# Performance work log

Measured on AMD Instinct MI355X. Metric: run time of the kernel, lower is better.

## Reference

```python
import jax, jax.numpy as jnp
import numpy as np

B, LQ, LKV, D = 8, 2048, 2048, 1024

def setup_inputs() -> dict:
    key = jax.random.key(0)
    k1, k2, k3, k4, k5, k6, k7 = jax.random.split(key, 7)
    s = 1.0 / np.sqrt(D)
    return {
        "query": jax.random.normal(k1, (B, LQ, D), jnp.float32),
        "key": jax.random.normal(k2, (B, LKV, D), jnp.float32),
        "value": jax.random.normal(k3, (B, LKV, D), jnp.float32),
        "Wq": jax.random.uniform(k4, (D, D), jnp.float32, -s, s),
        "bq": jax.random.uniform(k5, (D,), jnp.float32, -s, s),
        "Wk": jax.random.uniform(k6, (D, D), jnp.float32, -s, s),
        "bk": jax.random.uniform(k7, (D,), jnp.float32, -s, s),
        "scale_factor": 32,
        "dropout_p": 0,
    }

def reference(query, key, value, Wq, bq, Wk, bk, scale_factor, dropout_p):
    # q/k linear projections (torch Linear: x @ W^T + b); v is used raw per the source
    q = jnp.einsum("bld,ed->ble", query, Wq) + bq
    k = jnp.einsum("bld,ed->ble", key, Wk) + bk
    scores = jnp.einsum("bqd,bkd->bqk", q, k) / jnp.float32(scale_factor)
    attn = jax.nn.softmax(scores, axis=-1)
    # dropout_p == 0 -> identity (deterministic baseline)
    return jnp.einsum("bqk,bkd->bqd", attn, value)
```

## Files before the change

### kernel.cpp

```cpp
#include <hip/hip_runtime.h>

typedef __bf16 bf16;
typedef __attribute__((ext_vector_type(4))) __bf16 bf16x4;
typedef __attribute__((ext_vector_type(8))) __bf16 bf16x8;
typedef __attribute__((ext_vector_type(4))) float f32x4;

__device__ __forceinline__ void gload_lds16(const void* g, void* l) {
  __builtin_amdgcn_global_load_lds(
      (const __attribute__((address_space(1))) unsigned int*)(unsigned long long)g,
      (__attribute__((address_space(3))) unsigned int*)(unsigned long long)l,
      16, 0, 0);
}

__global__ void cast_f32_bf16(const float* __restrict__ in, bf16* __restrict__ out, int n4) {
  int i = blockIdx.x * blockDim.x + threadIdx.x;
  if (i >= n4) return;
  float4 v = reinterpret_cast<const float4*>(in)[i];
  bf16x4 o;
  o[0] = (bf16)v.x; o[1] = (bf16)v.y; o[2] = (bf16)v.z; o[3] = (bf16)v.w;
  reinterpret_cast<bf16x4*>(out)[i] = o;
}

__global__ void transpose_cast(const float* __restrict__ V, bf16* __restrict__ VT,
                               int rows, int cols) {
  __shared__ bf16 tile[64][65];
  const int b = blockIdx.z;
  const float* Vb = V + (long)b * rows * cols;
  bf16* VTb = VT + (long)b * rows * cols;
  const int d0 = blockIdx.x * 64;
  const int k0 = blockIdx.y * 64;
  const int t = threadIdx.x;
  const int r = t >> 4;
  const int c4 = (t & 15) * 4;
#pragma unroll
  for (int p = 0; p < 4; ++p) {
    float4 v = *reinterpret_cast<const float4*>(&Vb[(long)(k0 + p * 16 + r) * cols + d0 + c4]);
    tile[p * 16 + r][c4 + 0] = (bf16)v.x;
    tile[p * 16 + r][c4 + 1] = (bf16)v.y;
    tile[p * 16 + r][c4 + 2] = (bf16)v.z;
    tile[p * 16 + r][c4 + 3] = (bf16)v.w;
  }
  __syncthreads();
#pragma unroll
  for (int p = 0; p < 4; ++p) {
    const int dd = p * 16 + r;
    bf16x4 o;
    o[0] = tile[c4 + 0][dd];
    o[1] = tile[c4 + 1][dd];
    o[2] = tile[c4 + 2][dd];
    o[3] = tile[c4 + 3][dd];
    *reinterpret_cast<bf16x4*>(&VTb[(long)(d0 + dd) * rows + k0 + c4]) = o;
  }
}

__global__ void softmax_rows(bf16* __restrict__ S) {
  const long row = blockIdx.x;
  bf16* p = S + row * 2048;
  const int t = threadIdx.x;
  const int wid = t >> 6;
  const int lane = t & 63;
  bf16x8 v = *reinterpret_cast<bf16x8*>(p + t * 8);
  float f[8];
  float m = -3.0e38f;
#pragma unroll
  for (int j = 0; j < 8; ++j) { f[j] = (float)v[j]; m = fmaxf(m, f[j]); }
#pragma unroll
  for (int off = 32; off >= 1; off >>= 1) m = fmaxf(m, __shfl_xor(m, off));
  __shared__ float redm[4], reds[4];
  if (lane == 0) redm[wid] = m;
  __syncthreads();
  m = fmaxf(fmaxf(redm[0], redm[1]), fmaxf(redm[2], redm[3]));
  float s = 0.f;
#pragma unroll
  for (int j = 0; j < 8; ++j) { f[j] = __expf(f[j] - m); s += f[j]; }
#pragma unroll
  for (int off = 32; off >= 1; off >>= 1) s += __shfl_xor(s, off);
  if (lane == 0) reds[wid] = s;
  __syncthreads();
  s = reds[0] + reds[1] + reds[2] + reds[3];
  const float inv = 1.0f / s;
  bf16x8 o;
#pragma unroll
  for (int j = 0; j < 8; ++j) o[j] = (bf16)(f[j] * inv);
  *reinterpret_cast<bf16x8*>(p + t * 8) = o;
}


#define BARRIER __builtin_amdgcn_s_barrier()
#define LGKM0                                              \
  do {                                                     \
    asm volatile("s_waitcnt lgkmcnt(0)" ::: "memory");     \
    __builtin_amdgcn_sched_barrier(0);                     \
  } while (0)
#define VM0                                                \
  do {                                                     \
    asm volatile("s_waitcnt vmcnt(0)" ::: "memory");       \
    __builtin_amdgcn_sched_barrier(0);                     \
  } while (0)

#define STAGE_A(buf, ko)                                        \
  {                                                             \
    bf16* l_ = ldsd + (buf) * 32768;                            \
    const bf16* g_ = gA + (ko);                                 \
    gload_lds16(g_, l_);                                        \
    gload_lds16(g_ + rK64, l_ + 4096);                          \
    gload_lds16(g_ + rK128, l_ + 8192);                         \
    gload_lds16(g_ + rK128 + rK64, l_ + 12288);                 \
  }
#define STAGE_B(buf, ko)                                        \
  {                                                             \
    bf16* l_ = ldsd + (buf) * 32768 + 16384;                    \
    const bf16* g_ = gB + (ko);                                 \
    gload_lds16(g_, l_);                                        \
    gload_lds16(g_ + rK64, l_ + 4096);                          \
    gload_lds16(g_ + rK128, l_ + 8192);                         \
    gload_lds16(g_ + rK128 + rK64, l_ + 12288);                 \
  }

#define LOADA(buf, mq)                                                        \
  {                                                                           \
    const bf16* p_ = aBase + (buf) * 32768 + (mq) * 4096;                     \
    _Pragma("unroll") for (int m_ = 0; m_ < 4; ++m_) {                        \
      a[m_][0] = *reinterpret_cast<const bf16x8*>(p_ + m_ * 1024 + pk0);      \
      a[m_][1] = *reinterpret_cast<const bf16x8*>(p_ + m_ * 1024 + pk1);      \
    }                                                                         \
  }
#define LOADB(buf, nq)                                                        \
  {                                                                           \
    const bf16* p_ = bBase + (buf) * 32768 + (nq) * 2048;                     \
    _Pragma("unroll") for (int n_ = 0; n_ < 2; ++n_) {                        \
      b[(nq) * 2 + n_][0] = *reinterpret_cast<const bf16x8*>(p_ + n_ * 1024 + pk0); \
      b[(nq) * 2 + n_][1] = *reinterpret_cast<const bf16x8*>(p_ + n_ * 1024 + pk1); \
    }                                                                         \
  }

#define MFMAQ(mq, nq)                                                         \
  _Pragma("unroll") for (int m_ = 0; m_ < 4; ++m_)                            \
  _Pragma("unroll") for (int n_ = 0; n_ < 2; ++n_)                            \
  _Pragma("unroll") for (int ks_ = 0; ks_ < 2; ++ks_)                         \
      acc[(mq) * 4 + m_][(nq) * 2 + n_] =                                     \
          __builtin_amdgcn_mfma_f32_16x16x32_bf16(                            \
              a[m_][ks_], b[(nq) * 2 + n_][ks_],                              \
              acc[(mq) * 4 + m_][(nq) * 2 + n_], 0, 0, 0);

template <int MODE>
__global__ __launch_bounds__(512, 2)
void gemm_bt(const bf16* __restrict__ A, const bf16* __restrict__ Bm,
             const float* __restrict__ bias, void* __restrict__ Cvoid,
             const int* __restrict__ scale_ptr,
             int M, int N, int K, long sA, long sB, long sC) {
  __shared__ bf16 lds[2][2][2][128][64];
  const int t = threadIdx.x;
  const int lane = t & 63;
  const int wid = t >> 6;
  const int wm = wid >> 2;
  const int wn = wid & 3;
  (void)M;

  const int gx = gridDim.x, gy = gridDim.y;
  const int nwg = gx * gy * gridDim.z;
  int id = blockIdx.x + gx * (blockIdx.y + gy * blockIdx.z);
  {
    const int cpx = nwg >> 3;
    id = (id & 7) * cpx + (id >> 3);
  }
  const int bx = id % gx;
  const int by = (id / gx) % gy;
  const int bz = id / (gx * gy);

  const bf16* Ab = A + (long)bz * sA;
  const bf16* Bb = Bm + (long)bz * sB;
  const int tile_m = by * 256;
  const int tile_n = bx * 256;

  const int srow = t >> 3;
  const int skc = t & 7;
  const int soff = ((skc ^ (srow & 7)) << 3);
  const bf16* gA = Ab + (long)(tile_m + srow) * K + soff;
  const bf16* gB = Bb + (long)(tile_n + srow) * K + soff;
  const long rK64 = (long)K << 6;
  const long rK128 = (long)K << 7;
  bf16* const ldsd = &lds[0][0][0][0][0] + wid * 512;

  const int frow = lane & 15;
  const int pk0 = (((lane >> 4) ^ (lane & 7))) << 3;
  const int pk1 = (((4 | (lane >> 4)) ^ (lane & 7))) << 3;
  const bf16* aBase = &lds[0][0][wm][frow][0];
  const bf16* bBase = &lds[0][1][wn >> 1][(wn & 1) * 64 + frow][0];

  bf16x8 a[4][2], b[4][2];
  f32x4 acc[8][4] = {};

  STAGE_A(0, 0)
  STAGE_B(0, 0)
  VM0;
  BARRIER;

  const int NK = K >> 6;
  int c = 0;
  for (int kt = 0; kt < NK - 1; ++kt, c ^= 1) {
    const long ko = (long)(kt + 1) << 6;
    LOADA(c, 0)
    LOADB(c, 0)
    STAGE_A(c ^ 1, ko)
    BARRIER;
    LGKM0;
    __builtin_amdgcn_s_setprio(1);
    MFMAQ(0, 0)
    __builtin_amdgcn_s_setprio(0);
    BARRIER;
    LOADB(c, 1)
    STAGE_B(c ^ 1, ko)
    BARRIER;
    LGKM0;
    __builtin_amdgcn_s_setprio(1);
    MFMAQ(0, 1)
    __builtin_amdgcn_s_setprio(0);
    BARRIER;
    LOADA(c, 1)
    BARRIER;
    LGKM0;
    __builtin_amdgcn_s_setprio(1);
    MFMAQ(1, 0)
    __builtin_amdgcn_s_setprio(0);
    BARRIER;
    VM0;
    BARRIER;
    __builtin_amdgcn_s_setprio(1);
    MFMAQ(1, 1)
    __builtin_amdgcn_s_setprio(0);
  }
  LOADA(c, 0)
  LOADB(c, 0)
  LOADB(c, 1)
  MFMAQ(0, 0)
  MFMAQ(0, 1)
  LOADA(c, 1)
  MFMAQ(1, 0)
  MFMAQ(1, 1)

  float scl = 1.0f;
  if (MODE == 1) {
    const int iv = scale_ptr[0];
    const float fv = __int_as_float(iv);
    const float sv = (iv > 0 && iv < (1 << 20)) ? (float)iv : fv;
    scl = 1.0f / sv;
  }
  const int rb = tile_m + wm * 128 + ((lane >> 4) << 2);
  const int cb = tile_n + wn * 64 + (lane & 15);
  if (MODE == 2) {
    float* C = reinterpret_cast<float*>(Cvoid) + (long)bz * sC;
#pragma unroll
    for (int mf = 0; mf < 8; ++mf)
#pragma unroll
      for (int nf = 0; nf < 4; ++nf)
#pragma unroll
        for (int r = 0; r < 4; ++r)
          C[(long)(rb + mf * 16 + r) * N + (cb + nf * 16)] = acc[mf][nf][r];
  } else {
    bf16* C = reinterpret_cast<bf16*>(Cvoid) + (long)bz * sC;
#pragma unroll
    for (int nf = 0; nf < 4; ++nf) {
      const int col = cb + nf * 16;
      const float bv = (MODE == 0) ? bias[col] : 0.0f;
#pragma unroll
      for (int mf = 0; mf < 8; ++mf)
#pragma unroll
        for (int r = 0; r < 4; ++r)
          C[(long)(rb + mf * 16 + r) * N + col] = (bf16)(acc[mf][nf][r] * scl + bv);
    }
  }
}

extern "C" void kernel_launch(void* const* d_in, const int* in_sizes, int n_in,
                              void* d_out, int out_size, void* d_ws, size_t ws_size,
                              hipStream_t stream) {
  (void)in_sizes; (void)n_in; (void)out_size; (void)ws_size;
  const float* query = (const float*)d_in[0];
  const float* key   = (const float*)d_in[1];
  const float* value = (const float*)d_in[2];
  const float* Wq    = (const float*)d_in[3];
  const float* bq    = (const float*)d_in[4];
  const float* Wk    = (const float*)d_in[5];
  const float* bk    = (const float*)d_in[6];
  const int*   scale = (const int*)d_in[7];

  const int L = 2048, D = 1024;
  char* ws = (char*)d_ws;
  bf16* q_cast = (bf16*)ws;
  bf16* k_cast = q_cast + (long)16384 * 1024;
  bf16* S      = q_cast;
  bf16* Qp     = (bf16*)(ws + (size_t)67108864);
  bf16* Kp     = (bf16*)(ws + (size_t)100663296);
  bf16* VT     = (bf16*)(ws + (size_t)134217728);
  bf16* Wqb    = (bf16*)(ws + (size_t)167772160);
  bf16* Wkb    = (bf16*)(ws + (size_t)169869312);

  cast_f32_bf16<<<16384, 256, 0, stream>>>(query, q_cast, 4194304);
  cast_f32_bf16<<<16384, 256, 0, stream>>>(key,   k_cast, 4194304);
  cast_f32_bf16<<<1024,  256, 0, stream>>>(Wq, Wqb, 262144);
  cast_f32_bf16<<<1024,  256, 0, stream>>>(Wk, Wkb, 262144);
  transpose_cast<<<dim3(16, 32, 8), 256, 0, stream>>>(value, VT, 2048, 1024);

  gemm_bt<0><<<dim3(4, 64, 1), 512, 0, stream>>>(q_cast, Wqb, bq, Qp, nullptr,
                                                 16384, 1024, 1024, 0, 0, 0);
  gemm_bt<0><<<dim3(4, 64, 1), 512, 0, stream>>>(k_cast, Wkb, bk, Kp, nullptr,
                                                 16384, 1024, 1024, 0, 0, 0);
  gemm_bt<1><<<dim3(8, 8, 8), 512, 0, stream>>>(Qp, Kp, nullptr, S, scale,
                                                2048, 2048, 1024,
                                                (long)L * D, (long)L * D, (long)L * L);
  softmax_rows<<<16384, 256, 0, stream>>>(S);
  gemm_bt<2><<<dim3(4, 8, 8), 512, 0, stream>>>(S, VT, nullptr, d_out, nullptr,
                                                2048, 1024, 2048,
                                                (long)L * L, (long)D * L, (long)L * D);
}
```

Before: 289.0 us.

## Split GEMM K-tile into two 32-wide halves with finer-grained load/compute pipelining

Restructures the bf16 GEMM main loop so each 64-wide K tile is staged and consumed as two 32-wide halves for A and B separately, using partial vmcnt waits so later stages keep loading while earlier halves are computed. LDS layout changes from a swizzled 64-column layout to an unswizzled [8][256][32] layout, and fragment loads become one bf16x8 per operand per half. This aims to overlap global-to-LDS traffic with MFMA work and drop the full vmcnt(0) stall. The price is more barriers and the loss of the XOR swizzle, which may bring back LDS bank conflicts.

```diff
diff --git a/kernel.cpp b/kernel.cpp
--- a/kernel.cpp
+++ b/kernel.cpp
@@ -92,56 +92,38 @@
     asm volatile("s_waitcnt lgkmcnt(0)" ::: "memory");     \
     __builtin_amdgcn_sched_barrier(0);                     \
   } while (0)
+#define VM4                                                \
+  do {                                                     \
+    asm volatile("s_waitcnt vmcnt(4)" ::: "memory");       \
+    __builtin_amdgcn_sched_barrier(0);                     \
+  } while (0)
 #define VM0                                                \
   do {                                                     \
     asm volatile("s_waitcnt vmcnt(0)" ::: "memory");       \
     __builtin_amdgcn_sched_barrier(0);                     \
   } while (0)
 
-#define STAGE_A(buf, ko)                                        \
+#define STAGE(buf, op, kh, g_)                                  \
   {                                                             \
-    bf16* l_ = ldsd + (buf) * 32768;                            \
-    const bf16* g_ = gA + (ko);                                 \
-    gload_lds16(g_, l_);                                        \
-    gload_lds16(g_ + rK64, l_ + 4096);                          \
-    gload_lds16(g_ + rK128, l_ + 8192);                         \
-    gload_lds16(g_ + rK128 + rK64, l_ + 12288);                 \
-  }
-#define STAGE_B(buf, ko)                                        \
-  {                                                             \
-    bf16* l_ = ldsd + (buf) * 32768 + 16384;                    \
-    const bf16* g_ = gB + (ko);                                 \
-    gload_lds16(g_, l_);                                        \
-    gload_lds16(g_ + rK64, l_ + 4096);                          \
-    gload_lds16(g_ + rK128, l_ + 8192);                         \
-    gload_lds16(g_ + rK128 + rK64, l_ + 12288);                 \
-  }
-
-#define LOADA(buf, mq)                                                        \
-  {                                                                           \
-    const bf16* p_ = aBase + (buf) * 32768 + (mq) * 4096;                     \
-    _Pragma("unroll") for (int m_ = 0; m_ < 4; ++m_) {                        \
-      a[m_][0] = *reinterpret_cast<const bf16x8*>(p_ + m_ * 1024 + pk0);      \
-      a[m_][1] = *reinterpret_cast<const bf16x8*>(p_ + m_ * 1024 + pk1);      \
-    }                                                                         \
-  }
-#define LOADB(buf, nq)                                                        \
-  {                                                                           \
-    const bf16* p_ = bBase + (buf) * 32768 + (nq) * 2048;                     \
-    _Pragma("unroll") for (int n_ = 0; n_ < 2; ++n_) {                        \
-      b[(nq) * 2 + n_][0] = *reinterpret_cast<const bf16x8*>(p_ + n_ * 1024 + pk0); \
-      b[(nq) * 2 + n_][1] = *reinterpret_cast<const bf16x8*>(p_ + n_ * 1024 + pk1); \
-    }                                                                         \
-  }
-
-#define MFMAQ(mq, nq)                                                         \
-  _Pragma("unroll") for (int m_ = 0; m_ < 4; ++m_)                            \
-  _Pragma("unroll") for (int n_ = 0; n_ < 2; ++n_)                            \
-  _Pragma("unroll") for (int ks_ = 0; ks_ < 2; ++ks_)                         \
-      acc[(mq) * 4 + m_][(nq) * 2 + n_] =                                     \
-          __builtin_amdgcn_mfma_f32_16x16x32_bf16(                            \
-              a[m_][ks_], b[(nq) * 2 + n_][ks_],                              \
-              acc[(mq) * 4 + m_][(nq) * 2 + n_], 0, 0, 0);
+    bf16* l_ = ldsw + (((buf) * 2 + (op)) * 2 + (kh)) * 8192;   \
+    gload_lds16((g_), l_);                                      \
+    gload_lds16((g_) + rK128, l_ + 4096);                       \
+  }
+
+#define LOADA(buf, kh, mq)                                                     \
+  _Pragma("unroll") for (int m_ = 0; m_ < 4; ++m_)                             \
+      a[m_] = *reinterpret_cast<const bf16x8*>(                                \
+          aB + ((buf) * 4 + (kh)) * 8192 + (mq) * 2048 + m_ * 512);
+#define LOADB(buf, kh)                                                         \
+  _Pragma("unroll") for (int n_ = 0; n_ < 4; ++n_)                             \
+      b[n_] = *reinterpret_cast<const bf16x8*>(                                \
+          bB + ((buf) * 4 + 2 + (kh)) * 8192 + n_ * 512);
+
+#define MFMAP(mq)                                                              \
+  _Pragma("unroll") for (int m_ = 0; m_ < 4; ++m_)                             \
+  _Pragma("unroll") for (int n_ = 0; n_ < 4; ++n_)                             \
+      acc[(mq) * 4 + m_][n_] = __builtin_amdgcn_mfma_f32_16x16x32_bf16(        \
+          a[m_], b[n_], acc[(mq) * 4 + m_][n_], 0, 0, 0);
 
 template <int MODE>
 __global__ __launch_bounds__(512, 2)
@@ -149,7 +131,7 @@
              const float* __restrict__ bias, void* __restrict__ Cvoid,
              const int* __restrict__ scale_ptr,
              int M, int N, int K, long sA, long sB, long sC) {
-  __shared__ bf16 lds[2][2][2][128][64];
+  __shared__ bf16 lds[8][256][32];
   const int t = threadIdx.x;
   const int lane = t & 63;
   const int wid = t >> 6;
@@ -173,71 +155,85 @@
   const int tile_m = by * 256;
   const int tile_n = bx * 256;
 
-  const int srow = t >> 3;
-  const int skc = t & 7;
-  const int soff = ((skc ^ (srow & 7)) << 3);
+  const int srow = t >> 2;
+  const int soff = (t & 3) * 8;
   const bf16* gA = Ab + (long)(tile_m + srow) * K + soff;
   const bf16* gB = Bb + (long)(tile_n + srow) * K + soff;
-  const long rK64 = (long)K << 6;
   const long rK128 = (long)K << 7;
-  bf16* const ldsd = &lds[0][0][0][0][0] + wid * 512;
+  bf16* const ldsw = &lds[0][0][0] + wid * 512;
 
   const int frow = lane & 15;
-  const int pk0 = (((lane >> 4) ^ (lane & 7))) << 3;
-  const int pk1 = (((4 | (lane >> 4)) ^ (lane & 7))) << 3;
-  const bf16* aBase = &lds[0][0][wm][frow][0];
-  const bf16* bBase = &lds[0][1][wn >> 1][(wn & 1) * 64 + frow][0];
-
-  bf16x8 a[4][2], b[4][2];
+  const int fko = (lane >> 4) * 8;
+  const bf16* aB = &lds[0][0][0] + (wm * 128 + frow) * 32 + fko;
+  const bf16* bB = &lds[0][0][0] + (wn * 64 + frow) * 32 + fko;
+
+  bf16x8 a[4], b[4];
   f32x4 acc[8][4] = {};
 
-  STAGE_A(0, 0)
-  STAGE_B(0, 0)
-  VM0;
+  STAGE(0, 0, 0, gA)
+  STAGE(0, 1, 0, gB)
+  STAGE(0, 0, 1, gA + 32)
+  STAGE(0, 1, 1, gB + 32)
+  VM4;
   BARRIER;
 
   const int NK = K >> 6;
   int c = 0;
   for (int kt = 0; kt < NK - 1; ++kt, c ^= 1) {
     const long ko = (long)(kt + 1) << 6;
-    LOADA(c, 0)
     LOADB(c, 0)
-    STAGE_A(c ^ 1, ko)
+    LOADA(c, 0, 0)
+    STAGE(c ^ 1, 0, 0, gA + ko)
     BARRIER;
     LGKM0;
     __builtin_amdgcn_s_setprio(1);
-    MFMAQ(0, 0)
+    MFMAP(0)
     __builtin_amdgcn_s_setprio(0);
     BARRIER;
-    LOADB(c, 1)
-    STAGE_B(c ^ 1, ko)
+    LOADA(c, 0, 1)
+    STAGE(c ^ 1, 1, 0, gB + ko)
+    VM4;
     BARRIER;
     LGKM0;
     __builtin_amdgcn_s_setprio(1);
-    MFMAQ(0, 1)
+    MFMAP(1)
     __builtin_amdgcn_s_setprio(0);
     BARRIER;
-    LOADA(c, 1)
+    LOADB(c, 1)
+    LOADA(c, 1, 0)
+    STAGE(c ^ 1, 0, 1, gA + ko + 32)
     BARRIER;
     LGKM0;
     __builtin_amdgcn_s_setprio(1);
-    MFMAQ(1, 0)
+    MFMAP(0)
     __builtin_amdgcn_s_setprio(0);
     BARRIER;
-    VM0;
-    BARRIER;
+    LOADA(c, 1, 1)
+    STAGE(c ^ 1, 1, 1, gB + ko + 32)
+    VM4;
+    BARRIER;
+    LGKM0;
     __builtin_amdgcn_s_setprio(1);
-    MFMAQ(1, 1)
+    MFMAP(1)
     __builtin_amdgcn_s_setprio(0);
-  }
-  LOADA(c, 0)
+    BARRIER;
+  }
   LOADB(c, 0)
+  LOADA(c, 0, 0)
+  LGKM0;
+  MFMAP(0)
+  LOADA(c, 0, 1)
+  LGKM0;
+  MFMAP(1)
+  VM0;
+  BARRIER;
   LOADB(c, 1)
-  MFMAQ(0, 0)
-  MFMAQ(0, 1)
-  LOADA(c, 1)
-  MFMAQ(1, 0)
-  MFMAQ(1, 1)
+  LOADA(c, 1, 0)
+  LGKM0;
+  MFMAP(0)
+  LOADA(c, 1, 1)
+  LGKM0;
+  MFMAP(1)
 
   float scl = 1.0f;
   if (MODE == 1) {
```

Result: slower. 309.7 us (+7.2%).

## Fuse fp32-to-bf16 input cast into a merged Q/K projection GEMM

Applied to the files above, without the earlier changes.

Replaces the separate query/key cast kernels and two projection GEMMs with one gemm_proj kernel. It reads fp32 activations directly, converts them to bf16 in registers before the LDS store, and handles both Q and K through the z grid dimension. This removes the bf16 round trip of two 16M-element tensors through global memory and three kernel launches. In exchange the new kernel uses a smaller 128x256 tile with K-step 32, which lowers MFMA work per synchronisation, and the fp32 A loads go through registers instead of direct-to-LDS loads.

```diff
diff --git a/kernel.cpp b/kernel.cpp
--- a/kernel.cpp
+++ b/kernel.cpp
@@ -146,16 +146,14 @@
 template <int MODE>
 __global__ __launch_bounds__(512, 2)
 void gemm_bt(const bf16* __restrict__ A, const bf16* __restrict__ Bm,
-             const float* __restrict__ bias, void* __restrict__ Cvoid,
-             const int* __restrict__ scale_ptr,
-             int M, int N, int K, long sA, long sB, long sC) {
+             void* __restrict__ Cvoid, const int* __restrict__ scale_ptr,
+             int N, int K, long sA, long sB, long sC) {
   __shared__ bf16 lds[2][2][2][128][64];
   const int t = threadIdx.x;
   const int lane = t & 63;
   const int wid = t >> 6;
   const int wm = wid >> 2;
   const int wn = wid & 3;
-  (void)M;
 
   const int gx = gridDim.x, gy = gridDim.y;
   const int nwg = gx * gy * gridDim.z;
@@ -262,13 +260,126 @@
 #pragma unroll
     for (int nf = 0; nf < 4; ++nf) {
       const int col = cb + nf * 16;
-      const float bv = (MODE == 0) ? bias[col] : 0.0f;
 #pragma unroll
       for (int mf = 0; mf < 8; ++mf)
 #pragma unroll
         for (int r = 0; r < 4; ++r)
-          C[(long)(rb + mf * 16 + r) * N + col] = (bf16)(acc[mf][nf][r] * scl + bv);
+          C[(long)(rb + mf * 16 + r) * N + col] = (bf16)(acc[mf][nf][r] * scl);
     }
+  }
+}
+
+__global__ __launch_bounds__(512, 2)
+void gemm_proj(const float* __restrict__ Aq, const float* __restrict__ Ak,
+               const bf16* __restrict__ Wb, const float* __restrict__ bias0,
+               const float* __restrict__ bias1, bf16* __restrict__ Cout,
+               int N, int K, long sB, long sC) {
+  __shared__ bf16 lds[2][12288];
+  const int t = threadIdx.x;
+  const int lane = t & 63;
+  const int wid = t >> 6;
+  const int wm = wid >> 2;
+  const int wn = wid & 3;
+
+  const int gx = gridDim.x, gy = gridDim.y;
+  const int nwg = gx * gy * gridDim.z;
+  int id = blockIdx.x + gx * (blockIdx.y + gy * blockIdx.z);
+  {
+    const int cpx = nwg >> 3;
+    id = (id & 7) * cpx + (id >> 3);
+  }
+  const int bx = id % gx;
+  const int by = (id / gx) % gy;
+  const int bz = id / (gx * gy);
+
+  const float* Af = bz ? Ak : Aq;
+  const bf16* Bb = Wb + (long)bz * sB;
+  const int tile_m = by * 128;
+  const int tile_n = bx * 256;
+
+  const int arow = t >> 2;
+  const int akc = t & 3;
+  const float* gAf = Af + (long)(tile_m + arow) * K + akc * 8;
+  bf16* const wA = &lds[0][0] + arow * 32 + (((akc ^ ((t >> 3) & 3))) << 3);
+
+  const int srow = t >> 2;
+  const int soff = (((t & 3) ^ ((t >> 3) & 3)) << 3);
+  const bf16* gB = Bb + (long)(tile_n + srow) * K + soff;
+  const long rK128 = (long)K << 7;
+  bf16* const ldsB = &lds[0][4096] + wid * 512;
+
+  const int frow = lane & 15;
+  const int pko = (((lane >> 4) ^ ((lane >> 1) & 3)) << 3);
+  const bf16* aB = &lds[0][0] + (wm * 64 + frow) * 32 + pko;
+  const bf16* bB = &lds[0][4096] + (wn * 64 + frow) * 32 + pko;
+
+  bf16x8 a[4], b[4];
+  f32x4 acc[4][4] = {};
+
+  {
+    float4 p0 = *reinterpret_cast<const float4*>(gAf);
+    float4 p1 = *reinterpret_cast<const float4*>(gAf + 4);
+    gload_lds16(gB, ldsB);
+    gload_lds16(gB + rK128, ldsB + 4096);
+    bf16x8 w;
+    w[0] = (bf16)p0.x; w[1] = (bf16)p0.y; w[2] = (bf16)p0.z; w[3] = (bf16)p0.w;
+    w[4] = (bf16)p1.x; w[5] = (bf16)p1.y; w[6] = (bf16)p1.z; w[7] = (bf16)p1.w;
+    *reinterpret_cast<bf16x8*>(wA) = w;
+    __syncthreads();
+  }
+
+  const int NK = K >> 5;
+  int c = 0;
+  for (int kt = 0; kt < NK - 1; ++kt, c ^= 1) {
+    const long ko = (long)(kt + 1) << 5;
+    float4 n0 = *reinterpret_cast<const float4*>(gAf + ko);
+    float4 n1 = *reinterpret_cast<const float4*>(gAf + ko + 4);
+    gload_lds16(gB + ko, ldsB + (c ^ 1) * 12288);
+    gload_lds16(gB + ko + rK128, ldsB + (c ^ 1) * 12288 + 4096);
+#pragma unroll
+    for (int n_ = 0; n_ < 4; ++n_)
+      b[n_] = *reinterpret_cast<const bf16x8*>(bB + c * 12288 + n_ * 512);
+#pragma unroll
+    for (int m_ = 0; m_ < 4; ++m_)
+      a[m_] = *reinterpret_cast<const bf16x8*>(aB + c * 12288 + m_ * 512);
+#pragma unroll
+    for (int m_ = 0; m_ < 4; ++m_)
+#pragma unroll
+      for (int n_ = 0; n_ < 4; ++n_)
+        acc[m_][n_] = __builtin_amdgcn_mfma_f32_16x16x32_bf16(a[m_], b[n_], acc[m_][n_], 0, 0, 0);
+    {
+      bf16x8 w;
+      w[0] = (bf16)n0.x; w[1] = (bf16)n0.y; w[2] = (bf16)n0.z; w[3] = (bf16)n0.w;
+      w[4] = (bf16)n1.x; w[5] = (bf16)n1.y; w[6] = (bf16)n1.z; w[7] = (bf16)n1.w;
+      *reinterpret_cast<bf16x8*>(wA + (c ^ 1) * 12288) = w;
+    }
+    __syncthreads();
+  }
+#pragma unroll
+  for (int n_ = 0; n_ < 4; ++n_)
+    b[n_] = *reinterpret_cast<const bf16x8*>(bB + c * 12288 + n_ * 512);
+#pragma unroll
+  for (int m_ = 0; m_ < 4; ++m_)
+    a[m_] = *reinterpret_cast<const bf16x8*>(aB + c * 12288 + m_ * 512);
+#pragma unroll
+  for (int m_ = 0; m_ < 4; ++m_)
+#pragma unroll
+    for (int n_ = 0; n_ < 4; ++n_)
+      acc[m_][n_] = __builtin_amdgcn_mfma_f32_16x16x32_bf16(a[m_], b[n_], acc[m_][n_], 0, 0, 0);
+
+  const float* bias = bz ? bias1 : bias0;
+  const int rb = tile_m + wm * 64 + ((lane >> 4) << 2);
+  const int cb = tile_n + wn * 64 + (lane & 15);
+  bf16* C = Cout + (long)bz * sC;
+#pragma unroll
+  for (int nf = 0; nf < 4; ++nf) {
+    const int col = cb + nf * 16;
+    const float bv = bias[col];
+#pragma unroll
+    for (int mf = 0; mf < 4; ++mf)
+#pragma unroll
+      for (int r = 0; r < 4; ++r)
+        C[(long)(rb + mf * 16 + r) * N + col] = (bf16)(acc[mf][nf][r] + bv);
   }
 }
 
@@ -287,30 +398,24 @@
 
   const int L = 2048, D = 1024;
   char* ws = (char*)d_ws;
-  bf16* q_cast = (bf16*)ws;
-  bf16* k_cast = q_cast + (long)16384 * 1024;
-  bf16* S      = q_cast;
+  bf16* S      = (bf16*)ws;
   bf16* Qp     = (bf16*)(ws + (size_t)67108864);
   bf16* Kp     = (bf16*)(ws + (size_t)100663296);
   bf16* VT     = (bf16*)(ws + (size_t)134217728);
   bf16* Wqb    = (bf16*)(ws + (size_t)167772160);
   bf16* Wkb    = (bf16*)(ws + (size_t)169869312);
 
-  cast_f32_bf16<<<16384, 256, 0, stream>>>(query, q_cast, 4194304);
-  cast_f32_bf16<<<16384, 256, 0, stream>>>(key,   k_cast, 4194304);
-  cast_f32_bf16<<<1024,  256, 0, stream>>>(Wq, Wqb, 262144);
-  cast_f32_bf16<<<1024,  256, 0, stream>>>(Wk, Wkb, 262144);
+  cast_f32_bf16<<<1024, 256, 0, stream>>>(Wq, Wqb, 262144);
+  cast_f32_bf16<<<1024, 256, 0, stream>>>(Wk, Wkb, 262144);
   transpose_cast<<<dim3(16, 32, 8), 256, 0, stream>>>(value, VT, 2048, 1024);
 
-  gemm_bt<0><<<dim3(4, 64, 1), 512, 0, stream>>>(q_cast, Wqb, bq, Qp, nullptr,
-                                                 16384, 1024, 1024, 0, 0, 0);
-  gemm_bt<0><<<dim3(4, 64, 1), 512, 0, stream>>>(k_cast, Wkb, bk, Kp, nullptr,
-                                                 16384, 1024, 1024, 0, 0, 0);
-  gemm_bt<1><<<dim3(8, 8, 8), 512, 0, stream>>>(Qp, Kp, nullptr, S, scale,
-                                                2048, 2048, 1024,
+  gemm_proj<<<dim3(4, 128, 2), 512, 0, stream>>>(query, key, Wqb, bq, bk, Qp,
+                                                 1024, 1024, 1048576L, 16777216L);
+  gemm_bt<1><<<dim3(8, 8, 8), 512, 0, stream>>>(Qp, Kp, S, scale,
+                                                2048, 1024,
                                                 (long)L * D, (long)L * D, (long)L * L);
   softmax_rows<<<16384, 256, 0, stream>>>(S);
-  gemm_bt<2><<<dim3(4, 8, 8), 512, 0, stream>>>(S, VT, nullptr, d_out, nullptr,
-                                                2048, 1024, 2048,
+  gemm_bt<2><<<dim3(4, 8, 8), 512, 0, stream>>>(S, VT, d_out, nullptr,
+                                                1024, 2048,
                                                 (long)L * L, (long)D * L, (long)L * D);
 }
```

New measurement: 296.8 us. 1.03x slower.
